# Kernel optimization log

Measured on AMD Instinct MI355X. Metric: run time of the kernel, lower is better.

The kernel has to match this reference:

```python
import jax, jax.numpy as jnp
import numpy as np

P = 4       # patch size
NQ = 6      # qubits (2**6 = 64 amplitudes)
NH = 8      # classic attention heads
HD = 8      # head dim (64 / 8)
EPS = 1e-9

_SIGNS = (1.0 - 2.0 * (((np.arange(64)[:, None] >> np.arange(NQ - 1, -1, -1)[None, :]) & 1))).astype(np.float32)  # [64, 6] Z-expectation signs, wire 0 = MSB


def _ln(x, g, b, eps=1e-5):
    m = x.mean(-1, keepdims=True)
    v = x.var(-1, keepdims=True)
    return (x - m) / jnp.sqrt(v + eps) * g + b


def _rot_rx(t):
    c = jnp.cos(t / 2).astype(jnp.complex64)
    s = jnp.sin(t / 2).astype(jnp.complex64)
    return jnp.stack([jnp.stack([c, -1j * s]), jnp.stack([-1j * s, c])])


def _rot_ry(t):
    c = jnp.cos(t / 2).astype(jnp.complex64)
    s = jnp.sin(t / 2).astype(jnp.complex64)
    return jnp.stack([jnp.stack([c, -s]), jnp.stack([s, c])])


def _apply_1q(psi, g, wire):
    # psi: [bsz, 2,2,2,2,2,2]; apply 2x2 unitary g on one wire
    ax = wire + 1
    psi = jnp.moveaxis(psi, ax, -1)
    psi = jnp.einsum('ab,...b->...a', g, psi)
    return jnp.moveaxis(psi, -1, ax)


def _cnot(psi, i):
    # CNOT on adjacent wires [i, i+1]
    cax = i + 1
    p0 = jnp.take(psi, 0, axis=cax)
    p1 = jnp.take(psi, 1, axis=cax)
    p1 = jnp.flip(p1, axis=cax)  # target axis i+2 shifts to cax after removing control axis
    return jnp.stack([p0, p1], axis=cax)


def _pqc(psi, w):
    # RX+RY -> CNOT chain -> RY per layer; w: [depth, NQ, 3]
    for l in range(w.shape[0]):
        for q in range(NQ):
            psi = _apply_1q(psi, _rot_rx(w[l, q, 0]), q)
            psi = _apply_1q(psi, _rot_ry(w[l, q, 1]), q)
        for q in range(NQ - 1):
            psi = _cnot(psi, q)
        for q in range(NQ):
            psi = _apply_1q(psi, _rot_ry(w[l, q, 2]), q)
    return psi


def _probs(psi):
    f = psi.reshape(psi.shape[0], 64)
    return f.real ** 2 + f.imag ** 2


def _measure_z(psi):
    return _probs(psi) @ jnp.asarray(_SIGNS)  # [bsz, 6]


def setup_inputs() -> dict:
    key = jax.random.key(0)
    k = lambda i: jax.random.fold_in(key, i)
    n = lambda i, shp, s=0.02: jax.random.normal(k(i), shp, jnp.float32) * s
    return dict(
        x=jax.random.normal(k(0), (16, 4, 128, 128), jnp.float32),
        conv_w=n(1, (384, 4, P, P)), conv_b=jnp.zeros((384,), jnp.float32),
        ln1_g=jnp.ones(64), ln1_b=jnp.zeros(64),
        wq=n(2, (64, 64)), wk=n(3, (64, 64)), wv=n(4, (64, 64)), wo=n(5, (64, 64)), bo=jnp.zeros(64),
        ln2_g=jnp.ones(64), ln2_b=jnp.zeros(64),
        enc_w=n(6, (2, NQ, 3), 0.1), q_w=n(7, (2, NQ, 3), 0.1), k_w=n(8, (2, NQ, 3), 0.1), v_w=n(9, (2, NQ, 3), 0.1),
        meas_q_w=n(10, (NQ, 3), 0.1), meas_k_w=n(11, (NQ, 3), 0.1), meas_v_w=n(12, (NQ, 3), 0.1),
        qproj_w=n(13, (4, NQ), 0.1), qproj_b=jnp.zeros(4),
        kproj_w=n(14, (4, NQ), 0.1), kproj_b=jnp.zeros(4),
        qkln_g=jnp.ones(4), qkln_b=jnp.zeros(4),
        raw_tau=jnp.asarray(np.log(np.exp(0.5) - 1.0), jnp.float32),
        inp_scale=jnp.ones(64),
        ln3_g=jnp.ones(64), ln3_b=jnp.zeros(64),
        mlp_w1=n(15, (256, 64)), mlp_b1=jnp.zeros(256), mlp_w2=n(16, (64, 256)), mlp_b2=jnp.zeros(64),
    )


def reference(x, conv_w, conv_b, ln1_g, ln1_b, wq, wk, wv, wo, bo, ln2_g, ln2_b,
              enc_w, q_w, k_w, v_w, meas_q_w, meas_k_w, meas_v_w,
              qproj_w, qproj_b, kproj_w, kproj_b, qkln_g, qkln_b, raw_tau, inp_scale,
              ln3_g, ln3_b, mlp_w1, mlp_b1, mlp_w2, mlp_b2):
    B, C, H, W = x.shape
    Hp, Wp = H // P, W // P
    L = Hp * Wp

    # --- PatchEmbed2D: DiT-style conv tokens [B, L, 384] ---
    t384 = jax.lax.conv_general_dilated(x, conv_w, (P, P), 'VALID',
                                        dimension_numbers=('NCHW', 'OIHW', 'NCHW'))
    t384 = t384.reshape(B, -1, L).transpose(0, 2, 1) + conv_b

    # --- PatchEmbed2D: unfold -> amplitude-normalized 64-d tokens ---
    t64 = x.reshape(B, C, Hp, P, Wp, P).transpose(0, 2, 4, 1, 3, 5).reshape(B, L, C * P * P)
    t64 = t64 / (jnp.linalg.norm(t64, axis=-1, keepdims=True) + EPS)

    # --- ClassicAttention64 (manual einsum + softmax MHSA) ---
    hin = _ln(t64, ln1_g, ln1_b)
    q = (hin @ wq.T).reshape(B, L, NH, HD).transpose(0, 2, 1, 3)
    kk = (hin @ wk.T).reshape(B, L, NH, HD).transpose(0, 2, 1, 3)
    v = (hin @ wv.T).reshape(B, L, NH, HD).transpose(0, 2, 1, 3)
    logits = jnp.einsum('bhid,bhjd->bhij', q, kk) * (HD ** -0.5)
    attn = jax.nn.softmax(logits, axis=-1)
    out = jnp.einsum('bhij,bhjd->bhid', attn, v).transpose(0, 2, 1, 3).reshape(B, L, 64)
    h = t64 + (out @ wo.T + bo)

    # --- QuantumAttention64 (QSANN, RBF kernel attention) ---
    xq = _ln(h, ln2_g, ln2_b) * inp_scale
    st = xq.reshape(B * L, 64)
    st = st / (jnp.linalg.norm(st, axis=-1, keepdims=True) + EPS)
    psi0 = st.astype(jnp.complex64).reshape((B * L,) + (2,) * NQ)
    psi_enc = _pqc(psi0, enc_w)
    zq = _measure_z(_pqc(_pqc(psi_enc, q_w), meas_q_w[None]))
    zk = _measure_z(_pqc(_pqc(psi_enc, k_w), meas_k_w[None]))
    pv = _probs(_pqc(_pqc(psi_enc, v_w), meas_v_w[None]))
    v64 = (pv / (pv.sum(-1, keepdims=True) + EPS)).reshape(B, L, 64)
    qv = _ln(zq @ qproj_w.T + qproj_b, qkln_g, qkln_b).reshape(B, L, -1)
    kv = _ln(zk @ kproj_w.T + kproj_b, qkln_g, qkln_b).reshape(B, L, -1)
    tau = jax.nn.softplus(raw_tau)
    d2 = jnp.maximum((qv ** 2).sum(-1)[:, :, None] + (kv ** 2).sum(-1)[:, None, :]
                     - 2.0 * jnp.einsum('bid,bjd->bij', qv, kv), 0.0)
    alpha = jnp.exp(-d2 / tau)
    wts = alpha / (alpha.sum(-1, keepdims=True) + EPS)
    h = h + jnp.einsum('bij,bjd->bid', wts, v64)

    # --- MLP (64 -> 256 -> 64, GELU) ---
    hm = _ln(h, ln3_g, ln3_b)
    h = h + (jax.nn.gelu(hm @ mlp_w1.T + mlp_b1, approximate=True) @ mlp_w2.T + mlp_b2)

    # combine both streams into a single output tensor [B, L, 448]
    return jnp.concatenate([t384, h], axis=-1)
```

## Files before the change

kernel.cpp:

```cpp
#include <hip/hip_runtime.h>

typedef float4 f4;
#define DEV static __device__ __forceinline__

constexpr int Ln = 1024;
constexpr float EPSn = 1e-9f;

typedef __attribute__((ext_vector_type(8))) short short8;
typedef __attribute__((ext_vector_type(16))) float f32x16;
typedef __attribute__((ext_vector_type(4))) unsigned int u32x4;

constexpr size_t OFF_T64 = 0;
constexpr size_t OFF_H   = 1048576;
constexpr size_t OFF_Q   = 2097152;
constexpr size_t OFF_K   = 3145728;
constexpr size_t OFF_V   = 4194304;
constexpr size_t OFF_AO  = 5242880;
constexpr size_t OFF_TR  = 6291456;
constexpr size_t OFF_WQT = OFF_TR + 24576;
constexpr size_t OFF_WKT = OFF_WQT + 4096;
constexpr size_t OFF_WVT = OFF_WKT + 4096;
constexpr size_t OFF_WOT = OFF_WVT + 4096;
constexpr size_t OFF_U   = OFF_WOT + 4096;
constexpr size_t OFF_W2P = OFF_U + 1024;
// ... 13 lines not shown
}

DEV float fast_exp2(float x) {
#if __has_builtin(__builtin_amdgcn_exp2f)
  return __builtin_amdgcn_exp2f(x);
#else
  return __expf(x * 0.6931471805599453f);
#endif
}

DEV void cmulc(float ar, float ai, float br, float bi, float& cr, float& ci) {
  cr = ar * br - ai * bi; ci = ar * bi + ai * br;
}
DEV void mat2mul(const float* A, const float* B, float* C) {
  for (int i = 0; i < 2; ++i)
    for (int j = 0; j < 2; ++j) {
      float sr = 0.f, si = 0.f;
      for (int kk = 0; kk < 2; ++kk) {
        float pr, pi;
        cmulc(A[(i * 2 + kk) * 2], A[(i * 2 + kk) * 2 + 1],
              B[(kk * 2 + j) * 2], B[(kk * 2 + j) * 2 + 1], pr, pi);
        sr += pr; si += pi;
      }
      C[(i * 2 + j) * 2] = sr; C[(i * 2 + j) * 2 + 1] = si;
    }
}

__global__ __launch_bounds__(256) void prep_all_kernel(
    const float* __restrict__ conv_w, const float* __restrict__ wq,
    const float* __restrict__ wk, const float* __restrict__ wv,
    const float* __restrict__ wo, const float* __restrict__ w1,
    const float* __restrict__ w2,
    const float* __restrict__ enc_w, const float* __restrict__ q_w,
    const float* __restrict__ k_w, const float* __restrict__ v_w,
    const float* __restrict__ mq, const float* __restrict__ mk,
    const float* __restrict__ mv, float* __restrict__ ws) {
  __shared__ float Ulds[288];
  int bx = blockIdx.x;
  int tid = threadIdx.x;
  if (bx < 288) {
    int g = bx * 256 + tid;
    if (g < 24576) {
      int kk = g / 384, o = g % 384;
      ws[OFF_TR + g] = conv_w[o * 64 + kk];
    } else if (g < 40960) {
      int i = g - 24576;
      int m = i >> 12;
      int r = i & 4095;
      int d = r >> 6, o = r & 63;
      const float* src = m == 0 ? wq : m == 1 ? wk : m == 2 ? wv : wo;
      ws[OFF_WQT + i] = src[o * 64 + d];
    } else if (g < 57344) {
      int i = g - 40960;
      int u4 = i >> 8, r = i & 255, o = r >> 2, j = r & 3;
      ws[OFF_W2P + i] = w2[o * 256 + u4 * 4 + j];
    } else if (g < 73728) {
      int i = g - 57344;
      int d4 = i >> 10, r = i & 1023, u = r >> 2, j = r & 3;
      ws[OFF_W1P + i] = w1[u * 64 + d4 * 4 + j];
    }
    return;
  }
  int ub = bx - 288;
  int branch = ub >> 2, quad = ub & 3;
  const float* bw = branch == 0 ? q_w : branch == 1 ? k_w : v_w;
  const float* mw = branch == 0 ? mq : branch == 1 ? mk : mv;
  if (tid < 36) {
    int blk = tid / 6, wire = tid % 6;
    auto W = [&](int l, int t) -> float {
      if (l <= 1) return enc_w[(l * 6 + wire) * 3 + t];
      if (l <= 3) return bw[((l - 2) * 6 + wire) * 3 + t];
      return mw[wire * 3 + t];
    };
    auto mk_rx = [](float th, float* M) {
      float c = cosf(0.5f * th), s = sinf(0.5f * th);
      M[0] = c; M[1] = 0; M[2] = 0; M[3] = -s; M[4] = 0; M[5] = -s; M[6] = c; M[7] = 0;
    };
    auto mk_ry = [](float th, float* M) {
      float c = cosf(0.5f * th), s = sinf(0.5f * th);
      M[0] = c; M[1] = 0; M[2] = -s; M[3] = 0; M[4] = s; M[5] = 0; M[6] = c; M[7] = 0;
    };
    float R[8];
    if (blk == 0) {
      float A[8], Bx[8];
      mk_ry(W(0, 1), A); mk_rx(W(0, 0), Bx);
      mat2mul(A, Bx, R);
    } else if (blk <= 4) {
      float A[8], Bx[8], C[8], T[8];
      mk_ry(W(blk, 1), A); mk_rx(W(blk, 0), Bx); mk_ry(W(blk - 1, 2), C);
      mat2mul(Bx, C, T); mat2mul(A, T, R);
    } else {
      mk_ry(W(4, 2), R);
    }
#pragma unroll
    for (int t = 0; t < 8; ++t) Ulds[(blk * 6 + wire) * 8 + t] = R[t];
  }
  __syncthreads();
  if (tid >= 64) return;
  int s = tid & 3;
  int lane = tid;
  int c = quad * 16 + (tid >> 2);
  bool bit1 = (s & 2) != 0;
  bool bit0 = (s & 1) != 0;
  float re[16], im[16];
#pragma unroll
  for (int i = 0; i < 16; ++i) { re[i] = (s * 16 + i == c) ? 1.f : 0.f; im[i] = 0.f; }
#pragma unroll 1
  for (int blk = 0; blk < 6; ++blk) {
    const float* Uw = Ulds + blk * 48;
    {
      const float* M = Uw;
      float cAr = bit1 ? M[6] : M[0], cAi = bit1 ? M[7] : M[1];
      float cBr = bit1 ? M[4] : M[2], cBi = bit1 ? M[5] : M[3];
#pragma unroll
      for (int i = 0; i < 16; ++i) {
        float pr = __shfl_xor(re[i], 2);
        float pi = __shfl_xor(im[i], 2);
        float nr = cAr * re[i] - cAi * im[i] + cBr * pr - cBi * pi;
        float ni = cAr * im[i] + cAi * re[i] + cBr * pi + cBi * pr;
        re[i] = nr; im[i] = ni;
      }
    }
    {
      const float* M = Uw + 8;
      float cAr = bit0 ? M[6] : M[0], cAi = bit0 ? M[7] : M[1];
      float cBr = bit0 ? M[4] : M[2], cBi = bit0 ? M[5] : M[3];
#pragma unroll
      for (int i = 0; i < 16; ++i) {
        float pr = __shfl_xor(re[i], 1);
        float pi = __shfl_xor(im[i], 1);
        float nr = cAr * re[i] - cAi * im[i] + cBr * pr - cBi * pi;
        float ni = cAr * im[i] + cAi * re[i] + cBr * pi + cBi * pr;
        re[i] = nr; im[i] = ni;
      }
    }
#pragma unroll
    for (int w = 2; w < 6; ++w) {
      const float* M = Uw + w * 8;
      const float m0 = M[0], m1 = M[1], m2 = M[2], m3 = M[3];
      const float m4 = M[4], m5 = M[5], m6 = M[6], m7 = M[7];
      const int mm = 8 >> (w - 2);
#pragma unroll
      for (int i = 0; i < 16; ++i) {
        if (i & mm) continue;
        int i1 = i | mm;
        float ar = re[i], ai = im[i], br = re[i1], bi = im[i1];
        re[i]  = m0 * ar - m1 * ai + m2 * br - m3 * bi;
        im[i]  = m0 * ai + m1 * ar + m2 * bi + m3 * br;
        re[i1] = m4 * ar - m5 * ai + m6 * br - m7 * bi;
        im[i1] = m4 * ai + m5 * ar + m6 * bi + m7 * br;
      }
    }
    if (blk < 5) {
      int sl = (lane & ~3) | (bit1 ? (s ^ 1) : s);
      float tr[16], ti[16];
#pragma unroll
      for (int i = 0; i < 16; ++i) {
        tr[i] = __shfl(re[i], sl);
        ti[i] = __shfl(im[i], sl);
      }
#pragma unroll
      for (int i = 0; i < 16; ++i) {
        int j = i;
        if (j & 2) j ^= 1;
        if (j & 4) j ^= 2;
        if (j & 8) j ^= 4;
        re[i] = bit0 ? tr[j ^ 8] : tr[j];
        im[i] = bit0 ? ti[j ^ 8] : ti[j];
      }
    }
  }
  float* dre = ws + OFF_UT + (size_t)branch * 8192 + c * 64 + s * 16;
  float* dim = dre + 4096;
#pragma unroll
  for (int i = 0; i < 16; i += 4) {
    f4 r4 = {re[i], re[i + 1], re[i + 2], re[i + 3]};
    f4 i4 = {im[i], im[i + 1], im[i + 2], im[i + 3]};
    *(f4*)(dre + i) = r4;
    *(f4*)(dim + i) = i4;
  }
}

__global__ __launch_bounds__(256) void patch_kernel(const float* __restrict__ x,
    const float* __restrict__ cwT, const float* __restrict__ conv_b,
    float* __restrict__ out, float* __restrict__ t64) {
  __shared__ float A[64][72];
  __shared__ float scl[64];
  int tid = threadIdx.x;
  int tb = blockIdx.x >> 1;
  int half = blockIdx.x & 1;
  int b = tb >> 4;
  int l0 = (tb & 15) << 6;
  int seg = tid & 15;
  int c = seg >> 2, ph = seg & 3;
#pragma unroll
  for (int r = 0; r < 4; ++r) {
    int tok = (tid >> 4) + (r << 4);
    int l = l0 + tok, hp = l >> 5, wp = l & 31;
    f4 v4 = *(const f4*)(x + (size_t)((b * 4 + c) * 128 + hp * 4 + ph) * 128 + wp * 4);
    A[seg * 4 + 0][tok] = v4.x;
    A[seg * 4 + 1][tok] = v4.y;
    A[seg * 4 + 2][tok] = v4.z;
    A[seg * 4 + 3][tok] = v4.w;
  }
  __syncthreads();
  if (tid < 64) {
    float ss = 0.f;
#pragma unroll
    for (int kk = 0; kk < 64; ++kk) { float vv = A[kk][tid]; ss += vv * vv; }
    scl[tid] = 1.0f / (sqrtf(ss) + EPSn);
  }
  __syncthreads();
  int t0 = tb << 6;
  if (half == 0) {
#pragma unroll
    for (int i = 0; i < 16; ++i) {
      int idx = tid + (i << 8);
      int tok = idx >> 6, kk = idx & 63;
      t64[(size_t)(t0 + tok) * 64 + kk] = A[kk][tok] * scl[tok];
    }
  }
  int tg = tid >> 4;
  int on = (tid & 15) + half * 16;
  float acc[4][12];
#pragma unroll
  for (int i = 0; i < 4; ++i)
#pragma unroll
    for (int jj = 0; jj < 12; ++jj) acc[i][jj] = 0.f;
  for (int kk = 0; kk < 64; ++kk) {
    float a[4];
#pragma unroll
    for (int i = 0; i < 4; ++i) a[i] = A[kk][tg * 4 + i];
    f4 w0 = *(const f4*)(cwT + kk * 384 + on * 12);
    f4 w1 = *(const f4*)(cwT + kk * 384 + on * 12 + 4);
    f4 w2 = *(const f4*)(cwT + kk * 384 + on * 12 + 8);
    float wv_[12] = {w0.x, w0.y, w0.z, w0.w, w1.x, w1.y, w1.z, w1.w, w2.x, w2.y, w2.z, w2.w};
#pragma unroll
    for (int i = 0; i < 4; ++i)
#pragma unroll
      for (int jj = 0; jj < 12; ++jj) acc[i][jj] += a[i] * wv_[jj];
  }
#pragma unroll
  for (int i = 0; i < 4; ++i) {
    int tok = tg * 4 + i;
    size_t basep = (size_t)(t0 + tok) * 448 + on * 12;
#pragma unroll
    for (int jj = 0; jj < 12; ++jj)
      out[basep + jj] = acc[i][jj] + conv_b[on * 12 + jj];
  }
}

__global__ __launch_bounds__(256) void qkv_kernel(const float* __restrict__ t64,
    const float* __restrict__ wqT, const float* __restrict__ wkT, const float* __restrict__ wvT,
    const float* __restrict__ g1, const float* __restrict__ b1,
    float* __restrict__ qo, float* __restrict__ ko, float* __restrict__ vo) {
  __shared__ float wS[12288];
  __shared__ float hin[16][64];
  int tid = threadIdx.x;
#pragma unroll
  for (int p = 0; p < 16; ++p) {
    int idx = p * 256 + tid;
    wS[idx] = wqT[idx];
    wS[4096 + idx] = wkT[idx];
    wS[8192 + idx] = wvT[idx];
  }
  int t0 = blockIdx.x << 4;
  int tt = tid >> 4, part = tid & 15;
  int t = t0 + tt;
  f4 xv = *(const f4*)(t64 + (size_t)t * 64 + part * 4);
  float mean = red16(xv.x + xv.y + xv.z + xv.w) * 0.015625f;
  float d0 = xv.x - mean, d1 = xv.y - mean, d2 = xv.z - mean, d3 = xv.w - mean;
  float var = red16(d0 * d0 + d1 * d1 + d2 * d2 + d3 * d3) * 0.015625f;
  float rs = rsqrtf(var + 1e-5f);
  f4 g4 = *(const f4*)(g1 + part * 4);
  f4 b4 = *(const f4*)(b1 + part * 4);
  f4 hh;
  hh.x = d0 * rs * g4.x + b4.x; hh.y = d1 * rs * g4.y + b4.y;
  hh.z = d2 * rs * g4.z + b4.z; hh.w = d3 * rs * g4.w + b4.w;
  *(f4*)&hin[tt][part * 4] = hh;
  __syncthreads();
  float qa0 = 0, qa1 = 0, qa2 = 0, qa3 = 0;
  float ka0 = 0, ka1 = 0, ka2 = 0, ka3 = 0;
  float va0 = 0, va1 = 0, va2 = 0, va3 = 0;
  for (int d = 0; d < 64; ++d) {
    float hd = hin[tt][d];
    f4 wq4 = *(const f4*)&wS[d * 64 + part * 4];
    f4 wk4 = *(const f4*)&wS[4096 + d * 64 + part * 4];
    f4 wv4 = *(const f4*)&wS[8192 + d * 64 + part * 4];
    qa0 += hd * wq4.x; qa1 += hd * wq4.y; qa2 += hd * wq4.z; qa3 += hd * wq4.w;
    ka0 += hd * wk4.x; ka1 += hd * wk4.y; ka2 += hd * wk4.z; ka3 += hd * wk4.w;
    va0 += hd * wv4.x; va1 += hd * wv4.y; va2 += hd * wv4.z; va3 += hd * wv4.w;
  }
  f4 qr = {qa0, qa1, qa2, qa3}, kr = {ka0, ka1, ka2, ka3}, vr = {va0, va1, va2, va3};
  *(f4*)(qo + (size_t)t * 64 + part * 4) = qr;
  *(f4*)(ko + (size_t)t * 64 + part * 4) = kr;
  *(f4*)(vo + (size_t)t * 64 + part * 4) = vr;
}

__global__ __launch_bounds__(256) void attn_kernel(const float* __restrict__ qg,
    const float* __restrict__ kg, const float* __restrict__ vg, float* __restrict__ ao) {
  __shared__ __align__(16) unsigned short Klds[Ln][8];
  __shared__ __align__(16) unsigned short Vt[10][1032];
  __shared__ __align__(16) unsigned short Qlds[128][8];
  int bh = blockIdx.x;
  int b = bh >> 3, hh = bh & 7;
  int tid = threadIdx.x;
  int qbase = (blockIdx.y << 7);
  const float* kb = kg + (size_t)(b * Ln) * 64 + hh * 8;
  const float* vb = vg + (size_t)(b * Ln) * 64 + hh * 8;
  const float* qb = qg + (size_t)(b * Ln + qbase) * 64 + hh * 8;
  const float SC = 0.51006944f;
#pragma unroll
  for (int p = 0; p < 8; ++p) {
    int e4 = p * 256 + tid;
    int j = e4 >> 1, part = e4 & 1;
    f4 kv = *(const f4*)(kb + (size_t)j * 64 + part * 4);
    *(uint2*)&Klds[j][part * 4] =
        make_uint2(pk_bf16(kv.x * SC, kv.y * SC), pk_bf16(kv.z * SC, kv.w * SC));
    f4 vv = *(const f4*)(vb + (size_t)j * 64 + part * 4);
    unsigned int u01 = pk_bf16(vv.x, vv.y), u23 = pk_bf16(vv.z, vv.w);
    int d0 = part * 4;
    Vt[d0 + 0][j] = (unsigned short)u01;
    Vt[d0 + 1][j] = (unsigned short)(u01 >> 16);
    Vt[d0 + 2][j] = (unsigned short)u23;
    Vt[d0 + 3][j] = (unsigned short)(u23 >> 16);
  }
#pragma unroll
  for (int p = 0; p < 4; ++p) {
    int j = p * 256 + tid;
    Vt[8][j] = 0x3F80;
    Vt[9][j] = 0;
  }
  {
    int j = tid >> 1, part = tid & 1;
    f4 qv = *(const f4*)(qb + (size_t)j * 64 + part * 4);
    *(uint2*)&Qlds[j][part * 4] = make_uint2(pk_bf16(qv.x, qv.y), pk_bf16(qv.z, qv.w));
  }
  __syncthreads();

  int l = tid & 63, w = tid >> 6;
  int lq = l & 31;
  bool lo = l < 32;
  const short8 zero8 = {0, 0, 0, 0, 0, 0, 0, 0};
  short8 qf = *(const short8*)&Qlds[w * 32 + lq][0];
  qf = lo ? qf : zero8;
  int d = lq;
  int dc = d > 9 ? 9 : d;
  int vrow0 = (l >> 5) * 8;
  f32x16 acc = {};
  const f32x16 fz = {};
  for (int t = 0; t < 32; ++t) {
    short8 kf = *(const short8*)&Klds[t * 32 + lq][0];
    kf = lo ? kf : zero8;
    f32x16 s = __builtin_amdgcn_mfma_f32_32x32x16_bf16(kf, qf, fz, 0, 0, 0);
    float p[16];
#pragma unroll
    for (int r = 0; r < 16; ++r) p[r] = fast_exp2(s[r]);
    unsigned int c0 = pk_bf16(p[0], p[1]),  c1 = pk_bf16(p[2], p[3]);
    unsigned int c2 = pk_bf16(p[4], p[5]),  c3 = pk_bf16(p[6], p[7]);
    unsigned int c4 = pk_bf16(p[8], p[9]),  c5 = pk_bf16(p[10], p[11]);
    unsigned int c6 = pk_bf16(p[12], p[13]), c7 = pk_bf16(p[14], p[15]);
    unsigned int x0 = c0, y0 = c2;
    asm("v_permlane32_swap_b32 %0, %1" : "+v"(x0), "+v"(y0));
    unsigned int x1 = c1, y1 = c3;
    asm("v_permlane32_swap_b32 %0, %1" : "+v"(x1), "+v"(y1));
    unsigned int x4 = c4, y4 = c6;
    asm("v_permlane32_swap_b32 %0, %1" : "+v"(x4), "+v"(y4));
    unsigned int x5 = c5, y5 = c7;
    asm("v_permlane32_swap_b32 %0, %1" : "+v"(x5), "+v"(y5));
    union { u32x4 u; short8 s8; } B0, B1;
    B0.u = (u32x4){x0, x1, y0, y1};
    B1.u = (u32x4){x4, x5, y4, y5};
    int jb = t * 32 + vrow0;
    short8 av0 = *(const short8*)&Vt[dc][jb];
    short8 av1 = *(const short8*)&Vt[dc][jb + 16];
    acc = __builtin_amdgcn_mfma_f32_32x32x16_bf16(av0, B0.s8, acc, 0, 0, 0);
    acc = __builtin_amdgcn_mfma_f32_32x32x16_bf16(av1, B1.s8, acc, 0, 0, 0);
  }
  float ssum = __shfl(acc[4], lq);
  float inv = 1.0f / ssum;
  f4 o = {acc[0] * inv, acc[1] * inv, acc[2] * inv, acc[3] * inv};
  float* dst = ao + (size_t)(b * Ln + qbase + w * 32 + lq) * 64 + hh * 8 + (lo ? 0 : 4);
  *(f4*)dst = o;
}

__global__ __launch_bounds__(256) void proj_st_kernel(float* __restrict__ t64st,
    const float* __restrict__ ao, const float* __restrict__ woT, const float* __restrict__ bo,
    const float* __restrict__ g2, const float* __restrict__ b2, const float* __restrict__ iscale,
    float* __restrict__ hB) {
  __shared__ float woS[4096];
  __shared__ float aos[16][64];
  int tid = threadIdx.x;
#pragma unroll
  for (int p = 0; p < 16; ++p) {
    int idx = p * 256 + tid;
    woS[idx] = woT[idx];
  }
  int t0 = blockIdx.x << 4;
  int tt = tid >> 4, part = tid & 15;
  int t = t0 + tt;
  *(f4*)&aos[tt][part * 4] = *(const f4*)(ao + (size_t)t * 64 + part * 4);
  __syncthreads();
  f4 acc;
  acc.x = bo[part * 4 + 0]; acc.y = bo[part * 4 + 1];
  acc.z = bo[part * 4 + 2]; acc.w = bo[part * 4 + 3];
  for (int d = 0; d < 64; ++d) {
    float ad = aos[tt][d];
    f4 w4 = *(const f4*)&woS[d * 64 + part * 4];
    acc.x += ad * w4.x; acc.y += ad * w4.y; acc.z += ad * w4.z; acc.w += ad * w4.w;
  }
  f4 tv = *(const f4*)(t64st + (size_t)t * 64 + part * 4);
  f4 hv = {tv.x + acc.x, tv.y + acc.y, tv.z + acc.z, tv.w + acc.w};
  *(f4*)(hB + (size_t)t * 64 + part * 4) = hv;
  float mean = red16(hv.x + hv.y + hv.z + hv.w) * 0.015625f;
  float d0 = hv.x - mean, d1 = hv.y - mean, d2 = hv.z - mean, d3 = hv.w - mean;
  float var = red16(d0 * d0 + d1 * d1 + d2 * d2 + d3 * d3) * 0.015625f;
  float rs = rsqrtf(var + 1e-5f);
  f4 g4 = *(const f4*)(g2 + part * 4);
  f4 b4 = *(const f4*)(b2 + part * 4);
  f4 is4 = *(const f4*)(iscale + part * 4);
  float x0 = (d0 * rs * g4.x + b4.x) * is4.x;
  float x1 = (d1 * rs * g4.y + b4.y) * is4.y;
  float x2 = (d2 * rs * g4.z + b4.z) * is4.z;
  float x3 = (d3 * rs * g4.w + b4.w) * is4.w;
  float nrm = sqrtf(red16(x0 * x0 + x1 * x1 + x2 * x2 + x3 * x3));
  float rn = 1.0f / (nrm + EPSn);
  f4 stv = {x0 * rn, x1 * rn, x2 * rn, x3 * rn};
  *(f4*)(t64st + (size_t)t * 64 + part * 4) = stv;
}

__global__ __launch_bounds__(256) void quantum_kernel(const float* __restrict__ st,
    const float* __restrict__ ut,
    const float* __restrict__ qproj_w, const float* __restrict__ qproj_b,
    const float* __restrict__ kproj_w, const float* __restrict__ kproj_b,
    const float* __restrict__ qkg, const float* __restrict__ qkb,
    float* __restrict__ qvb, float* __restrict__ kvb, float* __restrict__ v64) {
  __shared__ float smem[12288];
  int tid = threadIdx.x;
  int branch = blockIdx.y;
  int t0 = blockIdx.x << 6;
  const float* ub = ut + (size_t)branch * 8192;
#pragma unroll
  for (int p = 0; p < 16; ++p) {
    int idx = p * 256 + tid;
    smem[idx] = st[(size_t)t0 * 64 + idx];
    smem[4096 + idx] = ub[idx];
    smem[8192 + idx] = ub[4096 + idx];
  }
  __syncthreads();
  int o = tid & 63, tg = tid >> 6;
  float accre[16], accim[16];
#pragma unroll
  for (int i = 0; i < 16; ++i) { accre[i] = 0.f; accim[i] = 0.f; }
  for (int k4 = 0; k4 < 16; ++k4) {
    float ur[4], ui[4];
#pragma unroll
    for (int j = 0; j < 4; ++j) {
      ur[j] = smem[4096 + (k4 * 4 + j) * 64 + o];
      ui[j] = smem[8192 + (k4 * 4 + j) * 64 + o];
    }
#pragma unroll
    for (int tt = 0; tt < 16; ++tt) {
      f4 a = *(const f4*)&smem[(tg * 16 + tt) * 64 + k4 * 4];
      accre[tt] += a.x * ur[0] + a.y * ur[1] + a.z * ur[2] + a.w * ur[3];
      accim[tt] += a.x * ui[0] + a.y * ui[1] + a.z * ui[2] + a.w * ui[3];
    }
  }
  __syncthreads();
#pragma unroll
  for (int tt = 0; tt < 16; ++tt) {
    int t = tg * 16 + tt;
    smem[t * 65 + o] = accre[tt] * accre[tt] + accim[tt] * accim[tt];
  }
  __syncthreads();
  int s = tid & 3;
  int tokL = tid >> 2;
  int token = t0 + tokL;
  bool bit1 = (s & 2) != 0;
  bool bit0 = (s & 1) != 0;
  float p[16];
#pragma unroll
  for (int i = 0; i < 16; ++i) p[i] = smem[tokL * 65 + s * 16 + i];
  float lsum = 0.f;
#pragma unroll
  for (int i = 0; i < 16; ++i) lsum += p[i];
  if (branch == 2) {
    float tot = lsum;
    tot += __shfl_xor(tot, 1);
    tot += __shfl_xor(tot, 2);
    float rn = 1.0f / (tot + EPSn);
    float* dst = v64 + (size_t)token * 64 + s * 16;
#pragma unroll
    for (int i = 0; i < 16; i += 4) {
      f4 o4 = {p[i] * rn, p[i + 1] * rn, p[i + 2] * rn, p[i + 3] * rn};
      *(f4*)(dst + i) = o4;
    }
  } else {
    float lz[4] = {0.f, 0.f, 0.f, 0.f};
#pragma unroll
    for (int i = 0; i < 16; ++i) {
      lz[0] += (i & 8) ? -p[i] : p[i];
      lz[1] += (i & 4) ? -p[i] : p[i];
      lz[2] += (i & 2) ? -p[i] : p[i];
      lz[3] += (i & 1) ? -p[i] : p[i];
    }
    float z[6];
    float u0 = bit1 ? -lsum : lsum;
    u0 += __shfl_xor(u0, 1); u0 += __shfl_xor(u0, 2); z[0] = u0;
    float u1 = bit0 ? -lsum : lsum;
    u1 += __shfl_xor(u1, 1); u1 += __shfl_xor(u1, 2); z[1] = u1;
#pragma unroll
    for (int q = 0; q < 4; ++q) {
      float v = lz[q];
      v += __shfl_xor(v, 1); v += __shfl_xor(v, 2);
      z[2 + q] = v;
    }
    const float* pw = branch == 0 ? qproj_w : kproj_w;
    const float* pb = branch == 0 ? qproj_b : kproj_b;
    float pr4[4];
#pragma unroll
    for (int jj = 0; jj < 4; ++jj) {
      float a = pb[jj];
#pragma unroll
      for (int qq = 0; qq < 6; ++qq) a += z[qq] * pw[jj * 6 + qq];
      pr4[jj] = a;
    }
    float mean = (pr4[0] + pr4[1] + pr4[2] + pr4[3]) * 0.25f;
    float var = 0.f;
#pragma unroll
    for (int jj = 0; jj < 4; ++jj) { float dd = pr4[jj] - mean; var += dd * dd; }
    var *= 0.25f;
    float rs = rsqrtf(var + 1e-5f);
    if (s == 0) {
      f4 o4;
      o4.x = (pr4[0] - mean) * rs * qkg[0] + qkb[0];
      o4.y = (pr4[1] - mean) * rs * qkg[1] + qkb[1];
      o4.z = (pr4[2] - mean) * rs * qkg[2] + qkb[2];
      o4.w = (pr4[3] - mean) * rs * qkg[3] + qkb[3];
      *(f4*)((branch == 0 ? qvb : kvb) + (size_t)token * 4) = o4;
    }
  }
}

__global__ __launch_bounds__(256) void rbf_kernel(const float* __restrict__ qvb,
    const float* __restrict__ kvb, const float* __restrict__ v64,
    const float* __restrict__ raw_tau, float* __restrict__ pacc, float* __restrict__ pasum) {
  __shared__ __align__(16) unsigned short Vt[64][520];
  __shared__ __align__(16) unsigned short kvbs[512][8];
  __shared__ float kks[512];
  int tid = threadIdx.x;
  int q0 = blockIdx.x << 7;
  int b = q0 >> 10;
  int kc = blockIdx.y;
  float tau = log1pf(__expf(raw_tau[0]));
  const float L2E = 1.4426950408889634f;
// ... 128 lines not shown
    for (int tok = 0; tok < 16; ++tok) {
      const float* hr = hmS[tok];
      float a0 = 0.f, a1 = 0.f, a2 = 0.f, a3 = 0.f;
#pragma unroll
      for (int d = 0; d < 64; d += 4) {
        a0 += hr[d] * wrow[d];
        a1 += hr[d + 1] * wrow[d + 1];
        a2 += hr[d + 2] * wrow[d + 2];
        a3 += hr[d + 3] * wrow[d + 3];
      }
      float a = bias + ((a0 + a1) + (a2 + a3));
      float tz = 0.7978845608028654f * (a + 0.044715f * a * a * a);
      float e = __expf(2.0f * tz);
      float th = 1.0f - 2.0f / (e + 1.0f);
      hidS[tok][u] = 0.5f * a * (1.0f + th);
    }
  }
  __syncthreads();
  int o = tid & 63, tg = tid >> 6;
  f4 acc[4];
#pragma unroll
  for (int tt = 0; tt < 4; ++tt) acc[tt] = {0.f, 0.f, 0.f, 0.f};
#pragma unroll 4
  for (int u4 = 0; u4 < 64; ++u4) {
    f4 wv = *(const f4*)(w2p + u4 * 256 + o * 4);
#pragma unroll
    for (int tt = 0; tt < 4; ++tt) {
      f4 hv = *(const f4*)&hidS[tg * 4 + tt][u4 * 4];
      acc[tt].x += hv.x * wv.x; acc[tt].y += hv.y * wv.y;
      acc[tt].z += hv.z * wv.z; acc[tt].w += hv.w * wv.w;
    }
  }
  float bb = b2v[o];
#pragma unroll
  for (int tt = 0; tt < 4; ++tt) {
    int tok = tg * 4 + tt;
    float r = bb + ((acc[tt].x + acc[tt].y) + (acc[tt].z + acc[tt].w));
    out[(size_t)(t0 + tok) * 448 + 384 + o] = hS[tok][o] + r;
  }
}

extern "C" void kernel_launch(void* const* d_in, const int* in_sizes, int n_in,
                              void* d_out, int out_size, void* d_ws, size_t ws_size,
                              hipStream_t stream) {
  (void)in_sizes; (void)n_in; (void)out_size; (void)ws_size;
  const float* x       = (const float*)d_in[0];
  const float* conv_w  = (const float*)d_in[1];
  const float* conv_b  = (const float*)d_in[2];
  const float* ln1_g   = (const float*)d_in[3];
  const float* ln1_b   = (const float*)d_in[4];
  const float* wq      = (const float*)d_in[5];
  const float* wk      = (const float*)d_in[6];
  const float* wv      = (const float*)d_in[7];
  const float* wo      = (const float*)d_in[8];
  const float* bo      = (const float*)d_in[9];
  const float* ln2_g   = (const float*)d_in[10];
  const float* ln2_b   = (const float*)d_in[11];
  const float* enc_w   = (const float*)d_in[12];
  const float* q_w     = (const float*)d_in[13];
  const float* k_w     = (const float*)d_in[14];
  const float* v_w     = (const float*)d_in[15];
  const float* mq_w    = (const float*)d_in[16];
  const float* mk_w    = (const float*)d_in[17];
  const float* mv_w    = (const float*)d_in[18];
  const float* qproj_w = (const float*)d_in[19];
  const float* qproj_b = (const float*)d_in[20];
  const float* kproj_w = (const float*)d_in[21];
  const float* kproj_b = (const float*)d_in[22];
  const float* qkln_g  = (const float*)d_in[23];
  const float* qkln_b  = (const float*)d_in[24];
  const float* raw_tau = (const float*)d_in[25];
  const float* iscale  = (const float*)d_in[26];
  const float* ln3_g   = (const float*)d_in[27];
  const float* ln3_b   = (const float*)d_in[28];
  const float* mlp_w1  = (const float*)d_in[29];
  const float* mlp_b1  = (const float*)d_in[30];
  const float* mlp_w2  = (const float*)d_in[31];
  const float* mlp_b2  = (const float*)d_in[32];
  float* out = (float*)d_out;
  float* ws  = (float*)d_ws;

  prep_all_kernel<<<300, 256, 0, stream>>>(conv_w, wq, wk, wv, wo, mlp_w1, mlp_w2,
                                           enc_w, q_w, k_w, v_w, mq_w, mk_w, mv_w, ws);
  patch_kernel<<<512, 256, 0, stream>>>(x, ws + OFF_TR, conv_b, out, ws + OFF_T64);
  qkv_kernel<<<1024, 256, 0, stream>>>(ws + OFF_T64, ws + OFF_WQT, ws + OFF_WKT, ws + OFF_WVT,
                                       ln1_g, ln1_b, ws + OFF_Q, ws + OFF_K, ws + OFF_V);
  attn_kernel<<<dim3(128, 8), 256, 0, stream>>>(ws + OFF_Q, ws + OFF_K, ws + OFF_V, ws + OFF_AO);
  proj_st_kernel<<<1024, 256, 0, stream>>>(ws + OFF_T64, ws + OFF_AO, ws + OFF_WOT, bo,
                                           ln2_g, ln2_b, iscale, ws + OFF_H);
  quantum_kernel<<<dim3(256, 3), 256, 0, stream>>>(ws + OFF_T64, ws + OFF_UT,
                                                   qproj_w, qproj_b, kproj_w, kproj_b,
                                                   qkln_g, qkln_b,
                                                   ws + OFF_K, ws + OFF_K + 65536, ws + OFF_Q);
  rbf_kernel<<<dim3(128, 2), 256, 0, stream>>>(ws + OFF_K, ws + OFF_K + 65536, ws + OFF_Q,
                                               raw_tau, ws + OFF_V, ws + OFF_K + 131072);
  m0m1m2_kernel<<<1024, 256, 0, stream>>>(ws + OFF_H, ws + OFF_V, ws + OFF_K + 131072,
                                          ln3_g, ln3_b, ws + OFF_W1P, mlp_b1,
                                          ws + OFF_W2P, mlp_b2, out);
}
```

Before: 169.0 us.

## Fuse output projection and state prep into the quantum kernel

Merges proj_st_kernel into quantum_kernel. Each block recomputes the attention output projection, residual add, LayerNorm and normalization for its 64 tokens in shared memory, instead of writing the normalized state to global memory and reading it back. This removes one launch and a global round trip, but the projection work is now done three times, once per quantum branch (blockIdx.y). Only branch 0 writes the residual h buffer.

After: 174.1 us. +3.0%, slower.

```diff
diff --git a/kernel.cpp b/kernel.cpp
--- a/kernel.cpp
+++ b/kernel.cpp
@@ -421,52 +421,11 @@
   *(f4*)dst = o;
 }
 
-__global__ __launch_bounds__(256) void proj_st_kernel(float* __restrict__ t64st,
-    const float* __restrict__ ao, const float* __restrict__ woT, const float* __restrict__ bo,
-    const float* __restrict__ g2, const float* __restrict__ b2, const float* __restrict__ iscale,
-    float* __restrict__ hB) {
-  __shared__ float woS[4096];
-  __shared__ float aos[16][64];
-  int tid = threadIdx.x;
-#pragma unroll
-  for (int p = 0; p < 16; ++p) {
-    int idx = p * 256 + tid;
-    woS[idx] = woT[idx];
-  }
-  int t0 = blockIdx.x << 4;
-  int tt = tid >> 4, part = tid & 15;
-  int t = t0 + tt;
-  *(f4*)&aos[tt][part * 4] = *(const f4*)(ao + (size_t)t * 64 + part * 4);
-  __syncthreads();
-  f4 acc;
-  acc.x = bo[part * 4 + 0]; acc.y = bo[part * 4 + 1];
-  acc.z = bo[part * 4 + 2]; acc.w = bo[part * 4 + 3];
-  for (int d = 0; d < 64; ++d) {
-    float ad = aos[tt][d];
-    f4 w4 = *(const f4*)&woS[d * 64 + part * 4];
-    acc.x += ad * w4.x; acc.y += ad * w4.y; acc.z += ad * w4.z; acc.w += ad * w4.w;
-  }
-  f4 tv = *(const f4*)(t64st + (size_t)t * 64 + part * 4);
-  f4 hv = {tv.x + acc.x, tv.y + acc.y, tv.z + acc.z, tv.w + acc.w};
-  *(f4*)(hB + (size_t)t * 64 + part * 4) = hv;
-  float mean = red16(hv.x + hv.y + hv.z + hv.w) * 0.015625f;
-  float d0 = hv.x - mean, d1 = hv.y - mean, d2 = hv.z - mean, d3 = hv.w - mean;
-  float var = red16(d0 * d0 + d1 * d1 + d2 * d2 + d3 * d3) * 0.015625f;
-  float rs = rsqrtf(var + 1e-5f);
-  f4 g4 = *(const f4*)(g2 + part * 4);
-  f4 b4 = *(const f4*)(b2 + part * 4);
-  f4 is4 = *(const f4*)(iscale + part * 4);
-  float x0 = (d0 * rs * g4.x + b4.x) * is4.x;
-  float x1 = (d1 * rs * g4.y + b4.y) * is4.y;
-  float x2 = (d2 * rs * g4.z + b4.z) * is4.z;
-  float x3 = (d3 * rs * g4.w + b4.w) * is4.w;
-  float nrm = sqrtf(red16(x0 * x0 + x1 * x1 + x2 * x2 + x3 * x3));
-  float rn = 1.0f / (nrm + EPSn);
-  f4 stv = {x0 * rn, x1 * rn, x2 * rn, x3 * rn};
-  *(f4*)(t64st + (size_t)t * 64 + part * 4) = stv;
-}
-
-__global__ __launch_bounds__(256) void quantum_kernel(const float* __restrict__ st,
+__global__ __launch_bounds__(256) void projq_kernel(
+    const float* __restrict__ t64, const float* __restrict__ ao,
+    const float* __restrict__ woT, const float* __restrict__ bo,
+    const float* __restrict__ g2, const float* __restrict__ b2,
+    const float* __restrict__ iscale, float* __restrict__ hB,
     const float* __restrict__ ut,
     const float* __restrict__ qproj_w, const float* __restrict__ qproj_b,
     const float* __restrict__ kproj_w, const float* __restrict__ kproj_b,
@@ -476,13 +435,49 @@
   int tid = threadIdx.x;
   int branch = blockIdx.y;
   int t0 = blockIdx.x << 6;
+#pragma unroll
+  for (int p = 0; p < 16; ++p) smem[p * 256 + tid] = woT[p * 256 + tid];
+  int tt = tid >> 4, part = tid & 15;
+#pragma unroll 1
+  for (int pass = 0; pass < 4; ++pass) {
+    int t = t0 + pass * 16 + tt;
+    __syncthreads();
+    *(f4*)&smem[4096 + tt * 64 + part * 4] = *(const f4*)(ao + (size_t)t * 64 + part * 4);
+    __syncthreads();
+    f4 acc;
+    acc.x = bo[part * 4 + 0]; acc.y = bo[part * 4 + 1];
+    acc.z = bo[part * 4 + 2]; acc.w = bo[part * 4 + 3];
+    for (int d = 0; d < 64; ++d) {
+      float ad = smem[4096 + tt * 64 + d];
+      f4 w4 = *(const f4*)&smem[d * 64 + part * 4];
+      acc.x += ad * w4.x; acc.y += ad * w4.y; acc.z += ad * w4.z; acc.w += ad * w4.w;
+    }
+    f4 tv = *(const f4*)(t64 + (size_t)t * 64 + part * 4);
+    f4 hv = {tv.x + acc.x, tv.y + acc.y, tv.z + acc.z, tv.w + acc.w};
+    if (branch == 0) *(f4*)(hB + (size_t)t * 64 + part * 4) = hv;
+    float mean = red16(hv.x + hv.y + hv.z + hv.w) * 0.015625f;
+    float d0 = hv.x - mean, d1 = hv.y - mean, d2 = hv.z - mean, d3 = hv.w - mean;
+    float var = red16(d0 * d0 + d1 * d1 + d2 * d2 + d3 * d3) * 0.015625f;
+    float rs = rsqrtf(var + 1e-5f);
+    f4 g4 = *(const f4*)(g2 + part * 4);
+    f4 b4 = *(const f4*)(b2 + part * 4);
+    f4 is4 = *(const f4*)(iscale + part * 4);
+    float x0 = (d0 * rs * g4.x + b4.x) * is4.x;
+    float x1 = (d1 * rs * g4.y + b4.y) * is4.y;
+    float x2 = (d2 * rs * g4.z + b4.z) * is4.z;
+    float x3 = (d3 * rs * g4.w + b4.w) * is4.w;
+    float nrm = sqrtf(red16(x0 * x0 + x1 * x1 + x2 * x2 + x3 * x3));
+    float rn = 1.0f / (nrm + EPSn);
+    f4 stv = {x0 * rn, x1 * rn, x2 * rn, x3 * rn};
+    *(f4*)&smem[8192 + (pass * 16 + tt) * 64 + part * 4] = stv;
+  }
+  __syncthreads();
   const float* ub = ut + (size_t)branch * 8192;
 #pragma unroll
   for (int p = 0; p < 16; ++p) {
     int idx = p * 256 + tid;
-    smem[idx] = st[(size_t)t0 * 64 + idx];
-    smem[4096 + idx] = ub[idx];
-    smem[8192 + idx] = ub[4096 + idx];
+    smem[idx] = ub[idx];
+    smem[4096 + idx] = ub[4096 + idx];
   }
   __syncthreads();
   int o = tid & 63, tg = tid >> 6;
@@ -493,21 +488,21 @@
     float ur[4], ui[4];
 #pragma unroll
     for (int j = 0; j < 4; ++j) {
-      ur[j] = smem[4096 + (k4 * 4 + j) * 64 + o];
-      ui[j] = smem[8192 + (k4 * 4 + j) * 64 + o];
-    }
-#pragma unroll
-    for (int tt = 0; tt < 16; ++tt) {
-      f4 a = *(const f4*)&smem[(tg * 16 + tt) * 64 + k4 * 4];
-      accre[tt] += a.x * ur[0] + a.y * ur[1] + a.z * ur[2] + a.w * ur[3];
-      accim[tt] += a.x * ui[0] + a.y * ui[1] + a.z * ui[2] + a.w * ui[3];
-    }
-  }
-  __syncthreads();
-#pragma unroll
-  for (int tt = 0; tt < 16; ++tt) {
-    int t = tg * 16 + tt;
-    smem[t * 65 + o] = accre[tt] * accre[tt] + accim[tt] * accim[tt];
+      ur[j] = smem[(k4 * 4 + j) * 64 + o];
+      ui[j] = smem[4096 + (k4 * 4 + j) * 64 + o];
+    }
+#pragma unroll
+    for (int tt2 = 0; tt2 < 16; ++tt2) {
+      f4 a = *(const f4*)&smem[8192 + (tg * 16 + tt2) * 64 + k4 * 4];
+      accre[tt2] += a.x * ur[0] + a.y * ur[1] + a.z * ur[2] + a.w * ur[3];
+      accim[tt2] += a.x * ui[0] + a.y * ui[1] + a.z * ui[2] + a.w * ui[3];
+    }
+  }
+  __syncthreads();
+#pragma unroll
+  for (int tt2 = 0; tt2 < 16; ++tt2) {
+    int t = tg * 16 + tt2;
+    smem[t * 65 + o] = accre[tt2] * accre[tt2] + accim[tt2] * accim[tt2];
   }
   __syncthreads();
   int s = tid & 3;
@@ -806,12 +801,11 @@
   qkv_kernel<<<1024, 256, 0, stream>>>(ws + OFF_T64, ws + OFF_WQT, ws + OFF_WKT, ws + OFF_WVT,
                                        ln1_g, ln1_b, ws + OFF_Q, ws + OFF_K, ws + OFF_V);
   attn_kernel<<<dim3(128, 8), 256, 0, stream>>>(ws + OFF_Q, ws + OFF_K, ws + OFF_V, ws + OFF_AO);
-  proj_st_kernel<<<1024, 256, 0, stream>>>(ws + OFF_T64, ws + OFF_AO, ws + OFF_WOT, bo,
-                                           ln2_g, ln2_b, iscale, ws + OFF_H);
-  quantum_kernel<<<dim3(256, 3), 256, 0, stream>>>(ws + OFF_T64, ws + OFF_UT,
-                                                   qproj_w, qproj_b, kproj_w, kproj_b,
-                                                   qkln_g, qkln_b,
-                                                   ws + OFF_K, ws + OFF_K + 65536, ws + OFF_Q);
+  projq_kernel<<<dim3(256, 3), 256, 0, stream>>>(ws + OFF_T64, ws + OFF_AO, ws + OFF_WOT, bo,
+                                                 ln2_g, ln2_b, iscale, ws + OFF_H,
+                                                 ws + OFF_UT, qproj_w, qproj_b,
+                                                 kproj_w, kproj_b, qkln_g, qkln_b,
+                                                 ws + OFF_K, ws + OFF_K + 65536, ws + OFF_Q);
   rbf_kernel<<<dim3(128, 2), 256, 0, stream>>>(ws + OFF_K, ws + OFF_K + 65536, ws + OFF_Q,
                                                raw_tau, ws + OFF_V, ws + OFF_K + 131072);
   m0m1m2_kernel<<<1024, 256, 0, stream>>>(ws + OFF_H, ws + OFF_V, ws + OFF_K + 131072,
```

## Fuse patch embedding and LN+QKV projection into one kernel

Applied to the files above, without the earlier changes.

Merges the patch kernel and the QKV kernel so that each block's token tile, already held in shared memory, is layer-normed and projected to Q/K/V directly instead of being re-read from the t64 buffer. The two halves of each token tile split the work: one half computes Q, the other K and V, loading only the weights it needs. This removes one kernel launch and a global round trip of the normalized tokens. In exchange it uses more shared memory per block, leaves Q/K/V work unbalanced between halves, and runs the projection on 512 blocks instead of 1024, which may lower parallelism.

After: 163.2 us. -3.5%, faster.

```diff
diff --git a/kernel.cpp b/kernel.cpp
--- a/kernel.cpp
+++ b/kernel.cpp
@@ -119,13 +119,13 @@
     };
     float R[8];
     if (blk == 0) {
-      float A[8], Bx[8];
-      mk_ry(W(0, 1), A); mk_rx(W(0, 0), Bx);
-      mat2mul(A, Bx, R);
+      float Am[8], Bx[8];
+      mk_ry(W(0, 1), Am); mk_rx(W(0, 0), Bx);
+      mat2mul(Am, Bx, R);
     } else if (blk <= 4) {
-      float A[8], Bx[8], C[8], T[8];
-      mk_ry(W(blk, 1), A); mk_rx(W(blk, 0), Bx); mk_ry(W(blk - 1, 2), C);
-      mat2mul(Bx, C, T); mat2mul(A, T, R);
+      float Am[8], Bx[8], C[8], T[8];
+      mk_ry(W(blk, 1), Am); mk_rx(W(blk, 0), Bx); mk_ry(W(blk - 1, 2), C);
+      mat2mul(Bx, C, T); mat2mul(Am, T, R);
     } else {
       mk_ry(W(4, 2), R);
     }
@@ -218,16 +218,32 @@
   }
 }
 
-__global__ __launch_bounds__(256) void patch_kernel(const float* __restrict__ x,
+__global__ __launch_bounds__(256) void patchqkv_kernel(const float* __restrict__ x,
     const float* __restrict__ cwT, const float* __restrict__ conv_b,
-    float* __restrict__ out, float* __restrict__ t64) {
-  __shared__ float A[64][72];
+    const float* __restrict__ wqT, const float* __restrict__ wkT,
+    const float* __restrict__ wvT,
+    const float* __restrict__ g1, const float* __restrict__ b1,
+    float* __restrict__ out, float* __restrict__ t64,
+    float* __restrict__ qo, float* __restrict__ ko, float* __restrict__ vo) {
+  __shared__ float A[64][73];
   __shared__ float scl[64];
+  __shared__ float hinS[16][64];
+  __shared__ float wS[8192];
   int tid = threadIdx.x;
   int tb = blockIdx.x >> 1;
   int half = blockIdx.x & 1;
   int b = tb >> 4;
   int l0 = (tb & 15) << 6;
+  if (half == 0) {
+#pragma unroll
+    for (int p = 0; p < 16; ++p) wS[p * 256 + tid] = wqT[p * 256 + tid];
+  } else {
+#pragma unroll
+    for (int p = 0; p < 16; ++p) {
+      wS[p * 256 + tid] = wkT[p * 256 + tid];
+      wS[4096 + p * 256 + tid] = wvT[p * 256 + tid];
+    }
+  }
   int seg = tid & 15;
   int c = seg >> 2, ph = seg & 3;
 #pragma unroll
@@ -257,81 +273,83 @@
       t64[(size_t)(t0 + tok) * 64 + kk] = A[kk][tok] * scl[tok];
     }
   }
-  int tg = tid >> 4;
-  int on = (tid & 15) + half * 16;
-  float acc[4][12];
-#pragma unroll
-  for (int i = 0; i < 4; ++i)
-#pragma unroll
-    for (int jj = 0; jj < 12; ++jj) acc[i][jj] = 0.f;
-  for (int kk = 0; kk < 64; ++kk) {
-    float a[4];
-#pragma unroll
-    for (int i = 0; i < 4; ++i) a[i] = A[kk][tg * 4 + i];
-    f4 w0 = *(const f4*)(cwT + kk * 384 + on * 12);
-    f4 w1 = *(const f4*)(cwT + kk * 384 + on * 12 + 4);
-    f4 w2 = *(const f4*)(cwT + kk * 384 + on * 12 + 8);
-    float wv_[12] = {w0.x, w0.y, w0.z, w0.w, w1.x, w1.y, w1.z, w1.w, w2.x, w2.y, w2.z, w2.w};
+  {
+    int tg = tid >> 4;
+    int on = (tid & 15) + half * 16;
+    float acc[4][12];
 #pragma unroll
     for (int i = 0; i < 4; ++i)
 #pragma unroll
-      for (int jj = 0; jj < 12; ++jj) acc[i][jj] += a[i] * wv_[jj];
-  }
-#pragma unroll
-  for (int i = 0; i < 4; ++i) {
-    int tok = tg * 4 + i;
-    size_t basep = (size_t)(t0 + tok) * 448 + on * 12;
-#pragma unroll
-    for (int jj = 0; jj < 12; ++jj)
-      out[basep + jj] = acc[i][jj] + conv_b[on * 12 + jj];
-  }
-}
-
-__global__ __launch_bounds__(256) void qkv_kernel(const float* __restrict__ t64,
-    const float* __restrict__ wqT, const float* __restrict__ wkT, const float* __restrict__ wvT,
-    const float* __restrict__ g1, const float* __restrict__ b1,
-    float* __restrict__ qo, float* __restrict__ ko, float* __restrict__ vo) {
-  __shared__ float wS[12288];
-  __shared__ float hin[16][64];
-  int tid = threadIdx.x;
-#pragma unroll
-  for (int p = 0; p < 16; ++p) {
-    int idx = p * 256 + tid;
-    wS[idx] = wqT[idx];
-    wS[4096 + idx] = wkT[idx];
-    wS[8192 + idx] = wvT[idx];
-  }
-  int t0 = blockIdx.x << 4;
+      for (int jj = 0; jj < 12; ++jj) acc[i][jj] = 0.f;
+    for (int kk = 0; kk < 64; ++kk) {
+      float a[4];
+#pragma unroll
+      for (int i = 0; i < 4; ++i) a[i] = A[kk][tg * 4 + i];
+      f4 w0 = *(const f4*)(cwT + kk * 384 + on * 12);
+      f4 w1 = *(const f4*)(cwT + kk * 384 + on * 12 + 4);
+      f4 w2 = *(const f4*)(cwT + kk * 384 + on * 12 + 8);
+      float wv_[12] = {w0.x, w0.y, w0.z, w0.w, w1.x, w1.y, w1.z, w1.w,
+                       w2.x, w2.y, w2.z, w2.w};
+#pragma unroll
+      for (int i = 0; i < 4; ++i)
+#pragma unroll
+        for (int jj = 0; jj < 12; ++jj) acc[i][jj] += a[i] * wv_[jj];
+    }
+#pragma unroll
+    for (int i = 0; i < 4; ++i) {
+      int tok = tg * 4 + i;
+      size_t basep = (size_t)(t0 + tok) * 448 + on * 12;
+#pragma unroll
+      for (int jj = 0; jj < 12; ++jj)
+        out[basep + jj] = acc[i][jj] + conv_b[on * 12 + jj];
+    }
+  }
   int tt = tid >> 4, part = tid & 15;
-  int t = t0 + tt;
-  f4 xv = *(const f4*)(t64 + (size_t)t * 64 + part * 4);
-  float mean = red16(xv.x + xv.y + xv.z + xv.w) * 0.015625f;
-  float d0 = xv.x - mean, d1 = xv.y - mean, d2 = xv.z - mean, d3 = xv.w - mean;
-  float var = red16(d0 * d0 + d1 * d1 + d2 * d2 + d3 * d3) * 0.015625f;
-  float rs = rsqrtf(var + 1e-5f);
-  f4 g4 = *(const f4*)(g1 + part * 4);
-  f4 b4 = *(const f4*)(b1 + part * 4);
-  f4 hh;
-  hh.x = d0 * rs * g4.x + b4.x; hh.y = d1 * rs * g4.y + b4.y;
-  hh.z = d2 * rs * g4.z + b4.z; hh.w = d3 * rs * g4.w + b4.w;
-  *(f4*)&hin[tt][part * 4] = hh;
-  __syncthreads();
-  float qa0 = 0, qa1 = 0, qa2 = 0, qa3 = 0;
-  float ka0 = 0, ka1 = 0, ka2 = 0, ka3 = 0;
-  float va0 = 0, va1 = 0, va2 = 0, va3 = 0;
-  for (int d = 0; d < 64; ++d) {
-    float hd = hin[tt][d];
-    f4 wq4 = *(const f4*)&wS[d * 64 + part * 4];
-    f4 wk4 = *(const f4*)&wS[4096 + d * 64 + part * 4];
-    f4 wv4 = *(const f4*)&wS[8192 + d * 64 + part * 4];
-    qa0 += hd * wq4.x; qa1 += hd * wq4.y; qa2 += hd * wq4.z; qa3 += hd * wq4.w;
-    ka0 += hd * wk4.x; ka1 += hd * wk4.y; ka2 += hd * wk4.z; ka3 += hd * wk4.w;
-    va0 += hd * wv4.x; va1 += hd * wv4.y; va2 += hd * wv4.z; va3 += hd * wv4.w;
-  }
-  f4 qr = {qa0, qa1, qa2, qa3}, kr = {ka0, ka1, ka2, ka3}, vr = {va0, va1, va2, va3};
-  *(f4*)(qo + (size_t)t * 64 + part * 4) = qr;
-  *(f4*)(ko + (size_t)t * 64 + part * 4) = kr;
-  *(f4*)(vo + (size_t)t * 64 + part * 4) = vr;
+#pragma unroll 1
+  for (int pass = 0; pass < 4; ++pass) {
+    int tokL = pass * 16 + tt;
+    int t = t0 + tokL;
+    float sclv = scl[tokL];
+    float e0 = A[part * 4 + 0][tokL] * sclv;
+    float e1 = A[part * 4 + 1][tokL] * sclv;
+    float e2 = A[part * 4 + 2][tokL] * sclv;
+    float e3 = A[part * 4 + 3][tokL] * sclv;
+    float mean = red16(e0 + e1 + e2 + e3) * 0.015625f;
+    float d0 = e0 - mean, d1 = e1 - mean, d2 = e2 - mean, d3 = e3 - mean;
+    float var = red16(d0 * d0 + d1 * d1 + d2 * d2 + d3 * d3) * 0.015625f;
+    float rs = rsqrtf(var + 1e-5f);
+    f4 g4 = *(const f4*)(g1 + part * 4);
+    f4 b4 = *(const f4*)(b1 + part * 4);
+    f4 hh;
+    hh.x = d0 * rs * g4.x + b4.x; hh.y = d1 * rs * g4.y + b4.y;
+    hh.z = d2 * rs * g4.z + b4.z; hh.w = d3 * rs * g4.w + b4.w;
+    *(f4*)&hinS[tt][part * 4] = hh;
+    __syncthreads();
+    if (half == 0) {
+      float qa0 = 0, qa1 = 0, qa2 = 0, qa3 = 0;
+      for (int d = 0; d < 64; ++d) {
+        float hd = hinS[tt][d];
+        f4 w4 = *(const f4*)&wS[d * 64 + part * 4];
+        qa0 += hd * w4.x; qa1 += hd * w4.y; qa2 += hd * w4.z; qa3 += hd * w4.w;
+      }
+      f4 qr = {qa0, qa1, qa2, qa3};
+      *(f4*)(qo + (size_t)t * 64 + part * 4) = qr;
+    } else {
+      float ka0 = 0, ka1 = 0, ka2 = 0, ka3 = 0;
+      float va0 = 0, va1 = 0, va2 = 0, va3 = 0;
+      for (int d = 0; d < 64; ++d) {
+        float hd = hinS[tt][d];
+        f4 wk4 = *(const f4*)&wS[d * 64 + part * 4];
+        f4 wv4 = *(const f4*)&wS[4096 + d * 64 + part * 4];
+        ka0 += hd * wk4.x; ka1 += hd * wk4.y; ka2 += hd * wk4.z; ka3 += hd * wk4.w;
+        va0 += hd * wv4.x; va1 += hd * wv4.y; va2 += hd * wv4.z; va3 += hd * wv4.w;
+      }
+      f4 kr = {ka0, ka1, ka2, ka3}, vr = {va0, va1, va2, va3};
+      *(f4*)(ko + (size_t)t * 64 + part * 4) = kr;
+      *(f4*)(vo + (size_t)t * 64 + part * 4) = vr;
+    }
+    __syncthreads();
+  }
 }
 
 __global__ __launch_bounds__(256) void attn_kernel(const float* __restrict__ qg,
@@ -802,9 +820,10 @@
 
   prep_all_kernel<<<300, 256, 0, stream>>>(conv_w, wq, wk, wv, wo, mlp_w1, mlp_w2,
                                            enc_w, q_w, k_w, v_w, mq_w, mk_w, mv_w, ws);
-  patch_kernel<<<512, 256, 0, stream>>>(x, ws + OFF_TR, conv_b, out, ws + OFF_T64);
-  qkv_kernel<<<1024, 256, 0, stream>>>(ws + OFF_T64, ws + OFF_WQT, ws + OFF_WKT, ws + OFF_WVT,
-                                       ln1_g, ln1_b, ws + OFF_Q, ws + OFF_K, ws + OFF_V);
+  patchqkv_kernel<<<512, 256, 0, stream>>>(x, ws + OFF_TR, conv_b,
+                                           ws + OFF_WQT, ws + OFF_WKT, ws + OFF_WVT,
+                                           ln1_g, ln1_b, out, ws + OFF_T64,
+                                           ws + OFF_Q, ws + OFF_K, ws + OFF_V);
   attn_kernel<<<dim3(128, 8), 256, 0, stream>>>(ws + OFF_Q, ws + OFF_K, ws + OFF_V, ws + OFF_AO);
   proj_st_kernel<<<1024, 256, 0, stream>>>(ws + OFF_T64, ws + OFF_AO, ws + OFF_WOT, bo,
                                            ln2_g, ln2_b, iscale, ws + OFF_H);
```
